# Optimization experiments

Measured on AMD Instinct MI355X. Metric: run time of the kernel, lower is better.

The kernel has to match this reference:

```python
import jax, jax.numpy as jnp
import numpy as np

ALPHA = 0.25
GAMMA = 2
IGNORE_INDEX = 255
LOSS_WEIGHT = 1.0
NUM_CLASSES = 19


def setup_inputs() -> dict:
    key = jax.random.key(0)
    k1, k2 = jax.random.split(key)
    N, C, H, W = 4, NUM_CLASSES, 512, 512
    cls_score = jax.random.normal(k1, (N, C, H, W), dtype=jnp.float32)
    label = jax.random.randint(k2, (N, H, W), 0, NUM_CLASSES, dtype=jnp.int64)
    return {"cls_score": cls_score, "label": label}


def reference(cls_score, label):
    # _expand_onehot_labels: valid pixels get a one-hot channel vector
    valid = (label >= 0) & (label != IGNORE_INDEX)          # [N,H,W]
    safe_lab = jnp.where(valid, label, 0)
    onehot = jax.nn.one_hot(safe_lab, cls_score.shape[1], axis=1,
                            dtype=cls_score.dtype)          # [N,C,H,W]
    validf = valid.astype(cls_score.dtype)[:, None, :, :]   # [N,1,H,W]
    onehot = onehot * validf

    # Focal class weight. NOTE: the original torch code uses the RAW logits
    # (temp_pred = pred.cpu()), not sigmoid(pred), when computing the weight.
    x = cls_score
    class_weight = jnp.where(onehot == 1,
                             ALPHA * (1.0 - x) ** GAMMA,
                             ALPHA * x ** GAMMA)            # [N,C,H,W]

    # binary_cross_entropy_with_logits, reduction='none', weight=class_weight
    bce = jnp.maximum(x, 0) - x * onehot + jnp.log1p(jnp.exp(-jnp.abs(x)))
    loss = bce * class_weight

    # weight_reduce_loss with weight=valid_mask (expanded), reduction='mean'
    loss = (loss * validf).mean()
    return LOSS_WEIGHT * loss
```

## Files before the change

### kernel.cpp

```cpp
#include <hip/hip_runtime.h>
#include <math.h>


#define NC 19
#define IGNORE_INDEX 255
#define ALPHA 0.25f

typedef float f32x4 __attribute__((ext_vector_type(4)));
typedef int   i32x4 __attribute__((ext_vector_type(4)));

constexpr int NBATCH = 4;
constexpr int HW = 512 * 512;
constexpr int NQ = NBATCH * NC * (HW / 4);
constexpr int BLOCK = 256;
constexpr int GRID = 2048;
constexpr int TT = GRID * BLOCK;
constexpr int BLOCK2 = 1024;
constexpr float INV_TOTAL = 1.0f / (float)(NBATCH * NC * HW);

constexpr int   TSEG  = 256;
constexpr float TMAX  = 6.0f;
constexpr float TSCALE = (float)TSEG / TMAX;
constexpr float TH     = TMAX / (float)TSEG;
constexpr float UCLAMP = 5.9999f;

template <int NWAVE>
__device__ __forceinline__ float block_reduce(float v, float* smem) {
    #pragma unroll
    for (int off = 32; off > 0; off >>= 1)
        v += __shfl_down(v, off, 64);
    const int lane = threadIdx.x & 63;
    const int wid  = threadIdx.x >> 6;
    if (lane == 0) smem[wid] = v;
    __syncthreads();
    float s = 0.0f;
    if (threadIdx.x == 0) {
        #pragma unroll
        for (int i = 0; i < NWAVE; ++i) s += smem[i];
    }
    return s;
}

__device__ __forceinline__ float quad_loss(const f32x4 v, const i32x4 l4,
                                           const int c, const float2* tab) {
    float acc = 0.0f;
    #pragma unroll
    for (int j = 0; j < 4; ++j) {
        const float xv  = v[j];
        const int   lb  = l4[j];
        const bool  val = (lb >= 0) && (lb != IGNORE_INDEX);
        const bool  t   = (lb == c);

        const float uc = fminf(fabsf(xv), UCLAMP);
        const float g  = uc * TSCALE;
        const int   ii = (int)g;
        const float fr = g - (float)ii;
        const float2 ab = tab[ii];
        const float sp  = fmaf(ab.y, fr, ab.x);

        const float y   = t ? -xv : xv;
        const float d   = y + (t ? 1.0f : 0.0f);
        const float w   = (val ? ALPHA : 0.0f) * d * d;
        const float bce = fmaxf(y, 0.0f) + sp;
        acc = fmaf(bce, w, acc);
    }
    return acc;
}

__global__ __launch_bounds__(BLOCK, 8) void focal_partial(
        const f32x4* __restrict__ x,
        const i32x4* __restrict__ lab4,
        float*       __restrict__ partial) {
    __shared__ float2 tab[TSEG];
    {
        const int i  = threadIdx.x;
        const float u0 = (float)i * TH;
        const float q0 = log1pf(__expf(-u0));
        const float q1 = log1pf(__expf(-(u0 + TH)));
        tab[i] = make_float2(q0, q1 - q0);
    }
    __syncthreads();

    const int tid = blockIdx.x * BLOCK + threadIdx.x;

    float acc = 0.0f;
    for (int q = tid; q < NQ; q += 2 * TT) {
        const unsigned plane0 = (unsigned)q >> 16;
        const int      pixq0  = q & 65535;
        const unsigned n0     = plane0 / NC;
        const int      c0     = (int)(plane0 - n0 * NC);
        const f32x4    v0     = __builtin_nontemporal_load(x + q);
        const i32x4    l0     = lab4[((size_t)n0 << 16) + pixq0];

        const int q1i = q + TT;
        if (q1i < NQ) {
            const unsigned plane1 = (unsigned)q1i >> 16;
            const int      pixq1  = q1i & 65535;
            const unsigned n1     = plane1 / NC;
            const int      c1     = (int)(plane1 - n1 * NC);
            const f32x4    v1     = __builtin_nontemporal_load(x + q1i);
            const i32x4    l1     = lab4[((size_t)n1 << 16) + pixq1];
            acc += quad_loss(v0, l0, c0, tab);
            acc += quad_loss(v1, l1, c1, tab);
        } else {
            acc += quad_loss(v0, l0, c0, tab);
        }
    }

    __shared__ float smem[BLOCK / 64];
    const float s = block_reduce<BLOCK / 64>(acc, smem);
    if (threadIdx.x == 0) partial[blockIdx.x] = s;
}

__global__ __launch_bounds__(BLOCK2) void focal_finalize(
        const float* __restrict__ partial,
        float*       __restrict__ out) {
    float acc = 0.0f;
    for (int i = threadIdx.x; i < GRID; i += BLOCK2)
        acc += partial[i];
    __shared__ float smem[BLOCK2 / 64];
    const float s = block_reduce<BLOCK2 / 64>(acc, smem);
    if (threadIdx.x == 0) out[0] = s * INV_TOTAL;
}

extern "C" void kernel_launch(void* const* d_in, const int* in_sizes, int n_in,
                              void* d_out, int out_size, void* d_ws, size_t ws_size,
                              hipStream_t stream) {
    const f32x4* cls_score = (const f32x4*)d_in[0];
    const i32x4* lab4      = (const i32x4*)d_in[1];
    float* out     = (float*)d_out;
    float* partial = (float*)d_ws;

    focal_partial<<<GRID, BLOCK, 0, stream>>>(cls_score, lab4, partial);
    focal_finalize<<<1, BLOCK2, 0, stream>>>(partial, out);
}
```

Before: 22.55 us.

## Issue all eight quad loads per thread up front with exact-sized grid

Replaces the grid-stride paired loop with a fixed eight-quad-per-thread scheme where the grid is sized to cover the input exactly. All value and label loads are issued before any compute, with an empty asm barrier to keep them in flight together and raise memory-level parallelism. Launch bounds are relaxed to allow more registers, and the nontemporal load hint is dropped. The trade-off is lower occupancy and a dependence on the input size dividing evenly.

```diff
diff --git a/kernel.cpp b/kernel.cpp
--- a/kernel.cpp
+++ b/kernel.cpp
@@ -13,7 +13,8 @@
 constexpr int HW = 512 * 512;
 constexpr int NQ = NBATCH * NC * (HW / 4);
 constexpr int BLOCK = 256;
-constexpr int GRID = 2048;
+constexpr int QPT = 8;
+constexpr int GRID = NQ / (BLOCK * QPT);
 constexpr int TT = GRID * BLOCK;
 constexpr int BLOCK2 = 1024;
 constexpr float INV_TOTAL = 1.0f / (float)(NBATCH * NC * HW);
@@ -67,7 +68,7 @@
     return acc;
 }
 
-__global__ __launch_bounds__(BLOCK, 8) void focal_partial(
+__global__ __launch_bounds__(BLOCK, 4) void focal_partial(
         const f32x4* __restrict__ x,
         const i32x4* __restrict__ lab4,
         float*       __restrict__ partial) {
@@ -83,29 +84,38 @@
 
     const int tid = blockIdx.x * BLOCK + threadIdx.x;
 
-    float acc = 0.0f;
-    for (int q = tid; q < NQ; q += 2 * TT) {
-        const unsigned plane0 = (unsigned)q >> 16;
-        const int      pixq0  = q & 65535;
-        const unsigned n0     = plane0 / NC;
-        const int      c0     = (int)(plane0 - n0 * NC);
-        const f32x4    v0     = __builtin_nontemporal_load(x + q);
-        const i32x4    l0     = lab4[((size_t)n0 << 16) + pixq0];
+    int c_[QPT];
+    int li_[QPT];
+    #pragma unroll
+    for (int k = 0; k < QPT; ++k) {
+        const int      q     = tid + k * TT;
+        const unsigned plane = (unsigned)q >> 16;
+        const unsigned n     = plane / NC;
+        c_[k]  = (int)(plane - n * NC);
+        li_[k] = (int)((n << 16) + (q & 65535));
+    }
 
-        const int q1i = q + TT;
-        if (q1i < NQ) {
-            const unsigned plane1 = (unsigned)q1i >> 16;
-            const int      pixq1  = q1i & 65535;
-            const unsigned n1     = plane1 / NC;
-            const int      c1     = (int)(plane1 - n1 * NC);
-            const f32x4    v1     = __builtin_nontemporal_load(x + q1i);
-            const i32x4    l1     = lab4[((size_t)n1 << 16) + pixq1];
-            acc += quad_loss(v0, l0, c0, tab);
-            acc += quad_loss(v1, l1, c1, tab);
-        } else {
-            acc += quad_loss(v0, l0, c0, tab);
-        }
-    }
+    f32x4 v0 = x[tid + 0 * TT], v1 = x[tid + 1 * TT],
+          v2 = x[tid + 2 * TT], v3 = x[tid + 3 * TT],
+          v4 = x[tid + 4 * TT], v5 = x[tid + 5 * TT],
+          v6 = x[tid + 6 * TT], v7 = x[tid + 7 * TT];
+    i32x4 l0 = lab4[li_[0]], l1 = lab4[li_[1]],
+          l2 = lab4[li_[2]], l3 = lab4[li_[3]],
+          l4 = lab4[li_[4]], l5 = lab4[li_[5]],
+          l6 = lab4[li_[6]], l7 = lab4[li_[7]];
+    asm volatile("" : "+v"(v0), "+v"(v1), "+v"(v2), "+v"(v3),
+                      "+v"(v4), "+v"(v5), "+v"(v6), "+v"(v7),
+                      "+v"(l0), "+v"(l1), "+v"(l2), "+v"(l3),
+                      "+v"(l4), "+v"(l5), "+v"(l6), "+v"(l7));
+
+    float acc = quad_loss(v0, l0, c_[0], tab);
+    acc += quad_loss(v1, l1, c_[1], tab);
+    acc += quad_loss(v2, l2, c_[2], tab);
+    acc += quad_loss(v3, l3, c_[3], tab);
+    acc += quad_loss(v4, l4, c_[4], tab);
+    acc += quad_loss(v5, l5, c_[5], tab);
+    acc += quad_loss(v6, l6, c_[6], tab);
+    acc += quad_loss(v7, l7, c_[7], tab);
 
     __shared__ float smem[BLOCK / 64];
     const float s = block_reduce<BLOCK / 64>(acc, smem);
```

Measured after the change: 22.23 us. Within noise of the previous version (-1.4%).
